# Kernel tuning notes

Measured on AMD Instinct MI355X. Metric: run time of the kernel, lower is better.

The kernel has to match this reference:

```python
import jax, jax.numpy as jnp
import numpy as np

N = 50000      # nodes
E = 800000     # edges in adj1/adj2 (avg degree 16)
ED = 400000    # edges after edge-drop
IN = 256       # input feature dim
H = 128        # hidden
H2 = 256       # 2*hidden
GATE = 64


def _xavier(key, shape):
    fan_in, fan_out = shape[0], shape[1]
    lim = np.sqrt(6.0 / (fan_in + fan_out)).astype(np.float32)
    return jax.random.uniform(key, shape, jnp.float32, -lim, lim)


def setup_inputs() -> dict:
    key = jax.random.key(0)
    ks = jax.random.split(key, 20)
    d = {}
    d["x1"] = jax.random.normal(ks[0], (N, IN), jnp.float32)
    d["x2"] = jax.random.normal(ks[1], (N, IN), jnp.float32)
    d["adj1_row"] = jax.random.randint(ks[2], (E,), 0, N, jnp.int32)
    d["adj1_col"] = jax.random.randint(ks[3], (E,), 0, N, jnp.int32)
    d["adj1_val"] = jax.random.uniform(ks[4], (E,), jnp.float32)
    d["adj2_row"] = jax.random.randint(ks[5], (E,), 0, N, jnp.int32)
    d["adj2_col"] = jax.random.randint(ks[6], (E,), 0, N, jnp.int32)
    d["adj2_val"] = jax.random.uniform(ks[7], (E,), jnp.float32)
    d["drop_row"] = jax.random.randint(ks[8], (ED,), 0, N, jnp.int32)
    d["drop_col"] = jax.random.randint(ks[9], (ED,), 0, N, jnp.int32)
    d["drop_val"] = jax.random.uniform(ks[10], (ED,), jnp.float32)
    d["deg"] = jax.random.uniform(ks[11], (N, 1), jnp.float32)
    # GCN layer 0: Linear(IN -> 2H) no bias in fc, plus GCN bias + PReLU
    d["W0"] = _xavier(ks[12], (IN, H2))
    d["b0"] = jnp.zeros((H2,), jnp.float32)
    d["a0"] = jnp.full((1,), 0.25, jnp.float32)  # PReLU param
    # GCN layer 1: Linear(2H -> H)
    d["W1"] = _xavier(ks[13], (H2, H))
    d["b1"] = jnp.zeros((H,), jnp.float32)
    d["a1"] = jnp.full((1,), 0.25, jnp.float32)
    # MLP gate
    d["G1w"] = _xavier(ks[14], (H, GATE))
    d["G1b"] = jnp.zeros((GATE,), jnp.float32)
    d["G2w"] = _xavier(ks[15], (H, GATE))
    d["G2b"] = jnp.zeros((GATE,), jnp.float32)
    d["G3w"] = _xavier(ks[16], (2 * GATE + 1, 1))
    d["G3b"] = jnp.zeros((1,), jnp.float32)
    return d


def _spmm(row, col, val, x, n):
    # sparse adj @ x : gather source features, scale by edge value, scatter-add to rows
    return jax.ops.segment_sum(val[:, None] * x[col], row, num_segments=n)


def _prelu(x, a):
    return jnp.where(x >= 0, x, a * x)


def reference(x1, x2, adj1_row, adj1_col, adj1_val, adj2_row, adj2_col, adj2_val,
              drop_row, drop_col, drop_val, deg,
              W0, b0, a0, W1, b1, a1, G1w, G1b, G2w, G2b, G3w, G3b):
    n = x1.shape[0]

    def gcn(x, row, col, val, W, b, a):
        return _prelu(_spmm(row, col, val, x @ W, n) + b, a)

    def branch(x, row, col, val):
        h = jax.nn.relu(gcn(x, row, col, val, W0, b0, a0))
        return gcn(h, row, col, val, W1, b1, a1)

    # dropout on x1/x2 is identity in eval mode
    h1 = branch(x1, adj1_row, adj1_col, adj1_val)
    h2 = branch(x2, adj1_row, adj1_col, adj1_val)
    h3 = branch(x1, adj2_row, adj2_col, adj2_val)
    h4 = branch(x1, drop_row, drop_col, drop_val)

    # MLP gate on detached h1, h3, deg
    z1 = jax.lax.stop_gradient(h1) @ G1w + G1b
    z2 = jax.lax.stop_gradient(h3) @ G2w + G2b
    w = jnp.concatenate([z1, z2, jax.lax.stop_gradient(deg)], axis=1)
    beta = jax.nn.sigmoid(w @ G3w + G3b)
    return (h1, h2, h3, h4, beta)
```

## Files before the change

### kernel.cpp

```cpp
#include <hip/hip_runtime.h>
#include <hip/hip_bf16.h>

#define H2C 256
#define HDC 128
#define GATEC 64
#define FBSH 9
#define NBF 320
#define EPB 8192
#define EPBH 2048
#define CAPB 10240

typedef unsigned short ushort_t;
typedef unsigned long long ull_t;
typedef __attribute__((ext_vector_type(8))) __bf16 bf16x8;
typedef __attribute__((ext_vector_type(4))) float f32x4;

__device__ inline float bf2f(unsigned short v) {
    union { unsigned u; float f; } t; t.u = ((unsigned)v) << 16; return t.f;
}
__device__ inline unsigned short f2bf(float v) {
    __hip_bfloat16 b = __float2bfloat16(v);
    return *reinterpret_cast<unsigned short*>(&b);
}

__device__ inline void gload_lds16(const void* g, void* l) {
    __builtin_amdgcn_global_load_lds(
        (const __attribute__((address_space(1))) unsigned int*)g,
        (__attribute__((address_space(3))) unsigned int*)l, 16, 0, 0);
}

__global__ __launch_bounds__(256)
void gemm_bf16_mfma(const ushort_t* __restrict__ A, const ushort_t* __restrict__ BT,
                    ushort_t* __restrict__ C, int M, int Nn, int K)
{
    __shared__ ushort_t Alds[128 * 64];
    __shared__ ushort_t Blds[128 * 64];
    const int tid  = threadIdx.x;
    const int w    = tid >> 6;
    const int lane = tid & 63;
    const int wr   = w >> 1;
    const int wc   = w & 1;
    const int bm   = blockIdx.y * 128;
    const int bn   = blockIdx.x * 128;

    f32x4 acc[4][4] = {};

    for (int k0 = 0; k0 < K; k0 += 64) {
        #pragma unroll
        for (int i = 0; i < 4; ++i) {
            const int lin = i * 256 + tid;
            const int r = lin >> 3, p = lin & 7;
            int rm = bm + r; if (rm >= M) rm = M - 1;
            const ushort_t* ga = A + (size_t)rm * K + k0 + ((p ^ (r & 7)) << 3);
            gload_lds16(ga, &Alds[i * 2048 + w * 512]);
        }
        #pragma unroll
        for (int i = 0; i < 4; ++i) {
            const int lin = i * 256 + tid;
            const int r = lin >> 3, p = lin & 7;
            const ushort_t* gb = BT + (size_t)(bn + r) * K + k0 + ((p ^ (r & 7)) << 3);
            gload_lds16(gb, &Blds[i * 2048 + w * 512]);
        }
        __syncthreads();
        #pragma unroll
        for (int kk = 0; kk < 2; ++kk) {
            bf16x8 af[4], bfr[4];
            #pragma unroll
            for (int m = 0; m < 4; ++m) {
                const int r = wr * 64 + m * 16 + (lane & 15);
                const int s = kk * 4 + (lane >> 4);
                af[m] = *reinterpret_cast<const bf16x8*>(&Alds[r * 64 + ((s ^ (r & 7)) << 3)]);
            }
            #pragma unroll
            for (int n = 0; n < 4; ++n) {
                const int r = wc * 64 + n * 16 + (lane & 15);
                const int s = kk * 4 + (lane >> 4);
                bfr[n] = *reinterpret_cast<const bf16x8*>(&Blds[r * 64 + ((s ^ (r & 7)) << 3)]);
            }
            #pragma unroll
            for (int m = 0; m < 4; ++m)
                #pragma unroll
                for (int n = 0; n < 4; ++n)
                    acc[m][n] = __builtin_amdgcn_mfma_f32_16x16x32_bf16(
                        af[m], bfr[n], acc[m][n], 0, 0, 0);
        }
        __syncthreads();
    }

    #pragma unroll
    for (int m = 0; m < 4; ++m) {
        const int row0 = bm + wr * 64 + m * 16 + ((lane >> 4) << 2);
        #pragma unroll
        for (int n = 0; n < 4; ++n) {
            const int col = bn + wc * 64 + n * 16 + (lane & 15);
            #pragma unroll
            for (int q = 0; q < 4; ++q) {
                const int row = row0 + q;
                if (row < M) C[(size_t)row * Nn + col] = f2bf(acc[m][n][q]);
            }
        }
    }
}

__global__ __launch_bounds__(256)
void gemm_xw_f32(const float* __restrict__ X1, const float* __restrict__ X2,
                 const ushort_t* __restrict__ BT, ushort_t* __restrict__ C,
                 int M, int Nn, int K, int Mh)
{
    __shared__ float    Af[128 * 32];
    __shared__ ushort_t Blds[128 * 32];
    const int tid  = threadIdx.x;
    const int w    = tid >> 6;
    const int lane = tid & 63;
    const int wr   = w >> 1;
    const int wc   = w & 1;
    const int bm   = blockIdx.y * 128;
    const int bn   = blockIdx.x * 128;

    f32x4 acc[4][4] = {};

    for (int k0 = 0; k0 < K; k0 += 32) {
        #pragma unroll
        for (int i = 0; i < 4; ++i) {
            const int lin = i * 256 + tid;
            const int r = lin >> 3, q = lin & 7;
            int rm = bm + r; if (rm >= M) rm = M - 1;
            const float* src = ((rm < Mh) ? X1 + (size_t)rm * K
                                          : X2 + (size_t)(rm - Mh) * K)
                               + k0 + ((q ^ (r & 7)) << 2);
            gload_lds16(src, &Af[i * 1024 + w * 256]);
        }
        #pragma unroll
        for (int i = 0; i < 2; ++i) {
            const int lin = i * 256 + tid;
            const int r = lin >> 2, q = lin & 3;
            const ushort_t* gb = BT + (size_t)(bn + r) * K + k0 + ((q ^ (r & 3)) << 3);
            gload_lds16(gb, &Blds[i * 2048 + w * 512]);
        }
        __syncthreads();
        {
            bf16x8 af[4], bfr[4];
            #pragma unroll
            for (int m = 0; m < 4; ++m) {
                const int r = wr * 64 + m * 16 + (lane & 15);
                const int s = lane >> 4;
                const int rx = r & 7;
                const float4 fa = *reinterpret_cast<const float4*>(
                    &Af[r * 32 + (((2 * s) ^ rx) << 2)]);
                const float4 fb = *reinterpret_cast<const float4*>(
                    &Af[r * 32 + (((2 * s + 1) ^ rx) << 2)]);
                ushort_t t[8] = {f2bf(fa.x), f2bf(fa.y), f2bf(fa.z), f2bf(fa.w),
                                 f2bf(fb.x), f2bf(fb.y), f2bf(fb.z), f2bf(fb.w)};
                af[m] = *reinterpret_cast<bf16x8*>(t);
            }
            #pragma unroll
            for (int n = 0; n < 4; ++n) {
                const int r = wc * 64 + n * 16 + (lane & 15);
                const int s = lane >> 4;
                bfr[n] = *reinterpret_cast<const bf16x8*>(&Blds[r * 32 + ((s ^ (r & 3)) << 3)]);
            }
            #pragma unroll
            for (int m = 0; m < 4; ++m)
                #pragma unroll
                for (int n = 0; n < 4; ++n)
                    acc[m][n] = __builtin_amdgcn_mfma_f32_16x16x32_bf16(
                        af[m], bfr[n], acc[m][n], 0, 0, 0);
        }
        __syncthreads();
    }

    #pragma unroll
    for (int m = 0; m < 4; ++m) {
        const int row0 = bm + wr * 64 + m * 16 + ((lane >> 4) << 2);
        #pragma unroll
        for (int n = 0; n < 4; ++n) {
            const int col = bn + wc * 64 + n * 16 + (lane & 15);
            #pragma unroll
            for (int q = 0; q < 4; ++q) {
                const int row = row0 + q;
                if (row < M) C[(size_t)row * Nn + col] = f2bf(acc[m][n][q]);
            }
        }
    }
}

__global__ __launch_bounds__(256)
void transpose2_f2bf_kernel(const float* __restrict__ W0, const float* __restrict__ W1,
                            ushort_t* __restrict__ W0T, ushort_t* __restrict__ W1T)
{
    int i = blockIdx.x * blockDim.x + threadIdx.x;
    if (i < H2C * H2C) {
        const int c = i / H2C, r = i % H2C;
        W0T[(size_t)c * H2C + r] = f2bf(W0[(size_t)r * H2C + c]);
    } else {
        i -= H2C * H2C;
        if (i < H2C * HDC) {
            const int c = i / H2C, r = i % H2C;
            W1T[(size_t)c * H2C + r] = f2bf(W1[(size_t)r * HDC + c]);
        }
    }
}

__global__ __launch_bounds__(256)
void bucket_hist_kernel(const int* __restrict__ r0, const int* __restrict__ r1_,
                        const int* __restrict__ rD, int E, int ED, int N,
                        int* __restrict__ bcnt)
{
    __shared__ int h[NBF];
    const int tid = threadIdx.x;
    for (int t = tid; t < NBF; t += 256) h[t] = 0;
    __syncthreads();
    const long long tot = 2LL * E + ED;
    const long long base = (long long)blockIdx.x * EPBH;
    #pragma unroll
    for (int k = 0; k < EPBH / 256; ++k) {
        const long long i = base + k * 256 + tid;
        if (i < tot) {
            int vr;
            if (i < E)            vr = r0[i];
            else if (i < 2LL * E) vr = N + r1_[i - E];
            else                  vr = 2 * N + rD[i - 2LL * E];
            atomicAdd(&h[vr >> FBSH], 1);
        }
    }
    __syncthreads();
    for (int t = tid; t < NBF; t += 256)
        if (h[t]) atomicAdd(&bcnt[t], h[t]);
}

__global__ void scan_buckets_kernel(const int* __restrict__ bcnt, int nbu, int tot,
                                    int* __restrict__ boff, int* __restrict__ gcur,
                                    int* __restrict__ g, int NR)
{
    if (threadIdx.x == 0) {
        int acc = 0;
        for (int t = 0; t < nbu; ++t) { boff[t] = acc; gcur[t] = acc; acc += bcnt[t]; }
        boff[nbu] = acc;
        g[NR] = tot;
    }
}

__global__ __launch_bounds__(256)
void bucket_stage_kernel(const int* __restrict__ r0, const int* __restrict__ c0, const float* __restrict__ v0,
                         const int* __restrict__ r1, const int* __restrict__ c1, const float* __restrict__ v1,
                         const int* __restrict__ rD, const int* __restrict__ cD, const float* __restrict__ vD,
                         int E, int ED, int N,
                         int* __restrict__ gcur, ull_t* __restrict__ stg)
{
    __shared__ int hcnt[NBF];
    __shared__ int hbase[NBF];
    const int tid = threadIdx.x;
    for (int t = tid; t < NBF; t += 256) hcnt[t] = 0;
    __syncthreads();
    const long long tot = 2LL * E + ED;
    const long long base = (long long)blockIdx.x * EPB;
    #pragma unroll
    for (int k = 0; k < EPB / 256; ++k) {
        const long long i = base + k * 256 + tid;
        if (i < tot) {
            int vr;
            if (i < E)            vr = r0[i];
            else if (i < 2LL * E) vr = N + r1[i - E];
            else                  vr = 2 * N + rD[i - 2LL * E];
            atomicAdd(&hcnt[vr >> FBSH], 1);
        }
    }
    __syncthreads();
    for (int t = tid; t < NBF; t += 256) {
        const int c = hcnt[t];
        hbase[t] = c ? atomicAdd(&gcur[t], c) : 0;
        hcnt[t] = 0;
    }
    __syncthreads();
    #pragma unroll
    for (int k = 0; k < EPB / 256; ++k) {
        const long long i = base + k * 256 + tid;
        if (i < tot) {
            int vr, cc; float vv;
            if (i < E)            { vr = r0[i];                 cc = c0[i];            vv = v0[i]; }
            else if (i < 2LL * E) { vr = N + r1[i - E];         cc = c1[i - E];        vv = v1[i - E]; }
            else                  { vr = 2 * N + rD[i - 2LL * E]; cc = cD[i - 2LL * E]; vv = vD[i - 2LL * E]; }
            const int fb = vr >> FBSH;
            const int p = hbase[fb] + atomicAdd(&hcnt[fb], 1);
            stg[p] = ((ull_t)(unsigned)vr << 32) | ((unsigned)cc << 16) | f2bf(vv);
        }
    }
}

__global__ __launch_bounds__(256)
void sort_bucket_kernel(const int* __restrict__ boff, int NR,
                        const ull_t* __restrict__ stg,
                        int* __restrict__ g, unsigned* __restrict__ ecv)
{
    __shared__ int hcnt[512];
    __shared__ int hscan[512];
    __shared__ unsigned pay[CAPB];
    const int b = blockIdx.x;
    const int r0 = b << FBSH;
    if (r0 >= NR) return;
    int r1 = r0 + (1 << FBSH); if (r1 > NR) r1 = NR;
    const int nrows = r1 - r0;
    const int base = boff[b], end = boff[b + 1];
    const int bsz = end - base;
    const int tid = threadIdx.x;
    hcnt[tid] = 0; hcnt[tid + 256] = 0;
    __syncthreads();
    for (int i = base + tid; i < end; i += 256)
        atomicAdd(&hcnt[(int)(stg[i] >> 32) - r0], 1);
    __syncthreads();
    hscan[tid] = hcnt[tid]; hscan[tid + 256] = hcnt[tid + 256];
    __syncthreads();
    for (int o = 1; o < 512; o <<= 1) {
        const int a0 = (tid >= o) ? hscan[tid - o] : 0;
        const int a1 = (tid + 256 >= o) ? hscan[tid + 256 - o] : 0;
        __syncthreads();
        hscan[tid] += a0; hscan[tid + 256] += a1;
        __syncthreads();
    }
    if (tid < nrows)       g[r0 + tid]       = base + hscan[tid] - hcnt[tid];
    if (tid + 256 < nrows) g[r0 + tid + 256] = base + hscan[tid + 256] - hcnt[tid + 256];
    hcnt[tid]       = hscan[tid] - hcnt[tid];
    hcnt[tid + 256] = hscan[tid + 256] - hcnt[tid + 256];
    __syncthreads();
    if (bsz <= CAPB) {
        for (int i = base + tid; i < end; i += 256) {
            const ull_t t = stg[i];
            const int p = atomicAdd(&hcnt[(int)(t >> 32) - r0], 1);
            pay[p] = (unsigned)t;
        }
        __syncthreads();
        for (int i = tid; i < bsz; i += 256)
            ecv[base + i] = pay[i];
    } else {
        for (int i = base + tid; i < end; i += 256) {
            const ull_t t = stg[i];
            const int p = atomicAdd(&hcnt[(int)(t >> 32) - r0], 1);
            ecv[base + p] = (unsigned)t;
        }
    }
}

__global__ __launch_bounds__(256)
void spmm_f256(const int* __restrict__ rp, const unsigned* __restrict__ ecv,
               const ushort_t* __restrict__ X, ushort_t* __restrict__ Y,
               const float* __restrict__ bias, const float* __restrict__ ap, int n)
{
    const int r = blockIdx.x * 4 + (threadIdx.x >> 6);
    if (r >= n) return;
    const int lane = threadIdx.x & 63;
    const int half = lane >> 5;
    const int l    = lane & 31;
    const int s = rp[r], e = rp[r + 1];
    float acc[8] = {};
    #pragma unroll 4
    for (int j = s + half; j < e; j += 2) {
        const unsigned ev = ecv[j];
        const float v = bf2f((ushort_t)ev);
        const uint4 x = *reinterpret_cast<const uint4*>(X + (size_t)(ev >> 16) * H2C + l * 8);
        acc[0] += v * bf2f((ushort_t)x.x); acc[1] += v * bf2f((ushort_t)(x.x >> 16));
        acc[2] += v * bf2f((ushort_t)x.y); acc[3] += v * bf2f((ushort_t)(x.y >> 16));
        acc[4] += v * bf2f((ushort_t)x.z); acc[5] += v * bf2f((ushort_t)(x.z >> 16));
        acc[6] += v * bf2f((ushort_t)x.w); acc[7] += v * bf2f((ushort_t)(x.w >> 16));
    }
    #pragma unroll
    for (int k = 0; k < 8; ++k) acc[k] += __shfl_xor(acc[k], 32);
    if (half == 0) {
        const float a = ap[0];
        const int f0 = l * 8;
        const float4 b0v = *reinterpret_cast<const float4*>(bias + f0);
        const float4 b1v = *reinterpret_cast<const float4*>(bias + f0 + 4);
        const float bb[8] = {b0v.x, b0v.y, b0v.z, b0v.w, b1v.x, b1v.y, b1v.z, b1v.w};
        unsigned o[4];
        #pragma unroll
        for (int k = 0; k < 8; k += 2) {
            float tx = acc[k] + bb[k];
            float ty = acc[k + 1] + bb[k + 1];
            tx = tx >= 0.f ? tx : a * tx;  ty = ty >= 0.f ? ty : a * ty;
            tx = fmaxf(tx, 0.f);           ty = fmaxf(ty, 0.f);
            o[k >> 1] = ((unsigned)f2bf(ty) << 16) | f2bf(tx);
        }
        *reinterpret_cast<uint4*>(Y + (size_t)r * H2C + f0) = make_uint4(o[0], o[1], o[2], o[3]);
    }
}

__global__ __launch_bounds__(256)
void spmm_f128(const int* __restrict__ rp, const unsigned* __restrict__ ecv,
               const ushort_t* __restrict__ X, float* __restrict__ Y,
               const float* __restrict__ bias, const float* __restrict__ ap, int n)
{
    const int r = blockIdx.x * 4 + (threadIdx.x >> 6);
    if (r >= n) return;
    const int lane = threadIdx.x & 63;
    const int q = lane >> 4;
    const int l = lane & 15;
    const int s = rp[r], e = rp[r + 1];
    float acc[8] = {};
    #pragma unroll 4
    for (int j = s + q; j < e; j += 4) {
        const unsigned ev = ecv[j];
        const float v = bf2f((ushort_t)ev);
        const uint4 x = *reinterpret_cast<const uint4*>(X + (size_t)(ev >> 16) * HDC + l * 8);
        acc[0] += v * bf2f((ushort_t)x.x); acc[1] += v * bf2f((ushort_t)(x.x >> 16));
        acc[2] += v * bf2f((ushort_t)x.y); acc[3] += v * bf2f((ushort_t)(x.y >> 16));
        acc[4] += v * bf2f((ushort_t)x.z); acc[5] += v * bf2f((ushort_t)(x.z >> 16));
        acc[6] += v * bf2f((ushort_t)x.w); acc[7] += v * bf2f((ushort_t)(x.w >> 16));
    }
    #pragma unroll
    for (int k = 0; k < 8; ++k) {
        acc[k] += __shfl_xor(acc[k], 16);
        acc[k] += __shfl_xor(acc[k], 32);
    }
    if (q == 0) {
        const float a = ap[0];
        const int f0 = l * 8;
        const float4 b0v = *reinterpret_cast<const float4*>(bias + f0);
        const float4 b1v = *reinterpret_cast<const float4*>(bias + f0 + 4);
        const float bb[8] = {b0v.x, b0v.y, b0v.z, b0v.w, b1v.x, b1v.y, b1v.z, b1v.w};
        float o[8];
        #pragma unroll
        for (int k = 0; k < 8; ++k) {
            float t = acc[k] + bb[k];
            o[k] = t >= 0.f ? t : a * t;
        }
        *reinterpret_cast<float4*>(Y + (size_t)r * HDC + f0)     = make_float4(o[0], o[1], o[2], o[3]);
        *reinterpret_cast<float4*>(Y + (size_t)r * HDC + f0 + 4) = make_float4(o[4], o[5], o[6], o[7]);
    }
}

__global__ __launch_bounds__(256)
void spmm_f128b(const int* __restrict__ rp, const unsigned* __restrict__ ecv,
                const ushort_t* __restrict__ X, float* __restrict__ out,
                const float* __restrict__ bias, const float* __restrict__ ap,
                int n3, int N)
{
    const int r = blockIdx.x * 4 + (threadIdx.x >> 6);
    if (r >= n3) return;
    const int reg = (r >= 2 * N) ? 2 : ((r >= N) ? 1 : 0);
    const ushort_t* Xs = X + (size_t)reg * N * HDC;
    float* Y = out + (size_t)(reg ? r + N : r) * HDC;
    const int lane = threadIdx.x & 63;
    const int q = lane >> 4;
    const int l = lane & 15;
    const int s = rp[r], e = rp[r + 1];
    float acc[8] = {};
    #pragma unroll 4
    for (int j = s + q; j < e; j += 4) {
        const unsigned ev = ecv[j];
        const float v = bf2f((ushort_t)ev);
        const uint4 x = *reinterpret_cast<const uint4*>(Xs + (size_t)(ev >> 16) * HDC + l * 8);
        acc[0] += v * bf2f((ushort_t)x.x); acc[1] += v * bf2f((ushort_t)(x.x >> 16));
        acc[2] += v * bf2f((ushort_t)x.y); acc[3] += v * bf2f((ushort_t)(x.y >> 16));
        acc[4] += v * bf2f((ushort_t)x.z); acc[5] += v * bf2f((ushort_t)(x.z >> 16));
        acc[6] += v * bf2f((ushort_t)x.w); acc[7] += v * bf2f((ushort_t)(x.w >> 16));
    }
    #pragma unroll
    for (int k = 0; k < 8; ++k) {
        acc[k] += __shfl_xor(acc[k], 16);
        acc[k] += __shfl_xor(acc[k], 32);
    }
    if (q == 0) {
        const float a = ap[0];
        const int f0 = l * 8;
        const float4 b0v = *reinterpret_cast<const float4*>(bias + f0);
        const float4 b1v = *reinterpret_cast<const float4*>(bias + f0 + 4);
        const float bb[8] = {b0v.x, b0v.y, b0v.z, b0v.w, b1v.x, b1v.y, b1v.z, b1v.w};
        float o[8];
        #pragma unroll
        for (int k = 0; k < 8; ++k) {
            float t = acc[k] + bb[k];
            o[k] = t >= 0.f ? t : a * t;
        }
        *reinterpret_cast<float4*>(Y + f0)     = make_float4(o[0], o[1], o[2], o[3]);
        *reinterpret_cast<float4*>(Y + f0 + 4) = make_float4(o[4], o[5], o[6], o[7]);
    }
}

__global__ void gate_pre_kernel(const float* __restrict__ G1w, const float* __restrict__ G1b,
                                const float* __restrict__ G2w, const float* __restrict__ G2b,
                                const float* __restrict__ G3w, const float* __restrict__ G3b,
                                float* __restrict__ U)
{
    const int h = threadIdx.x;
    float s1 = 0.f, s2 = 0.f;
    for (int g = 0; g < GATEC; ++g) {
        s1 += G1w[h * GATEC + g] * G3w[g];
        s2 += G2w[h * GATEC + g] * G3w[GATEC + g];
    }
    U[h] = s1;
    U[HDC + h] = s2;
    if (h == 0) {
        float c = G3b[0];
        for (int g = 0; g < GATEC; ++g)
            c += G1b[g] * G3w[g] + G2b[g] * G3w[GATEC + g];
        U[2 * HDC] = c;
        U[2 * HDC + 1] = G3w[2 * GATEC];
    }
}

__global__ __launch_bounds__(256)
void beta_kernel(const float* __restrict__ h1, const float* __restrict__ h3,
                 const float* __restrict__ deg, const float* __restrict__ U,
                 float* __restrict__ beta, int n)
{
    const int i = blockIdx.x * blockDim.x + threadIdx.x;
    if (i >= n) return;
    const float c = U[2 * HDC], wd = U[2 * HDC + 1];
    float s = c + wd * deg[i];
    const float4* h1p = reinterpret_cast<const float4*>(h1 + (size_t)i * HDC);
    const float4* h3p = reinterpret_cast<const float4*>(h3 + (size_t)i * HDC);
    const float4* u1p = reinterpret_cast<const float4*>(U);
    const float4* u2p = reinterpret_cast<const float4*>(U + HDC);
    #pragma unroll 8
    for (int j = 0; j < HDC / 4; ++j) {
        const float4 a = h1p[j], b = u1p[j];
        s += a.x * b.x + a.y * b.y + a.z * b.z + a.w * b.w;
        const float4 a2 = h3p[j], b2 = u2p[j];
        s += a2.x * b2.x + a2.y * b2.y + a2.z * b2.z + a2.w * b2.w;
    }
    beta[i] = 1.f / (1.f + expf(-s));
}

extern "C" void kernel_launch(void* const* d_in, const int* in_sizes, int n_in,
                              void* d_out, int out_size, void* d_ws, size_t ws_size,
                              hipStream_t stream)
{
    const float* x1  = (const float*)d_in[0];
    const float* x2  = (const float*)d_in[1];
    const int*   a1r = (const int*)d_in[2];
    const int*   a1c = (const int*)d_in[3];
    const float* a1v = (const float*)d_in[4];
    const int*   a2r = (const int*)d_in[5];
    const int*   a2c = (const int*)d_in[6];
    const float* a2v = (const float*)d_in[7];
    const int*   dr  = (const int*)d_in[8];
    const int*   dc  = (const int*)d_in[9];
    const float* dv  = (const float*)d_in[10];
    const float* deg = (const float*)d_in[11];
    const float* W0  = (const float*)d_in[12];
    const float* b0  = (const float*)d_in[13];
    const float* a0  = (const float*)d_in[14];
    const float* W1  = (const float*)d_in[15];
    const float* b1  = (const float*)d_in[16];
    const float* a1p = (const float*)d_in[17];
    const float* G1w = (const float*)d_in[18];
    const float* G1b = (const float*)d_in[19];
    const float* G2w = (const float*)d_in[20];
    const float* G2b = (const float*)d_in[21];
    const float* G3w = (const float*)d_in[22];
    const float* G3b = (const float*)d_in[23];

    const int E  = in_sizes[2];
    const int ED = in_sizes[8];
    const int N  = in_sizes[11];
    const int IN = in_sizes[0] / N;
    const long long TOT = 2LL * E + ED;
    const int NR  = 3 * N;
    const int NBUSED = (NR + (1 << FBSH) - 1) >> FBSH;

    auto pad = [](size_t b) { return (b + 255) & ~(size_t)255; };

    size_t need_b = pad((size_t)2 * N * H2C * 2)
                  + pad((size_t)3 * N * H2C * 2)
                  + pad((size_t)3 * N * HDC * 2)
                  + pad((size_t)H2C * H2C * 2) + pad((size_t)HDC * H2C * 2) + pad(258 * 4)
                  + pad((size_t)(NR + 1) * 4) + pad(NBF * 4) + pad((NBF + 1) * 4) + pad(NBF * 4)
                  + pad((size_t)TOT * 4)
                  + pad((size_t)TOT * 8);
    const bool batched = (ws_size >= need_b);

    char* base = (char*)d_ws;
    size_t off = 0;
    auto alloc = [&](size_t bytes) -> char* {
        char* p = base + off;
        off += (bytes + 255) & ~(size_t)255;
        return p;
    };
    ushort_t* XW12b = (ushort_t*)alloc((size_t)2 * N * H2C * 2);
    ull_t* stg; ushort_t *Bb, *Cb;
    if (batched) {
        char* R = alloc((size_t)3 * N * H2C * 2);
        Bb = (ushort_t*)R;
        Cb = (ushort_t*)alloc((size_t)3 * N * HDC * 2);
        stg = (ull_t*)alloc((size_t)TOT * 8);
    } else {
        char* R = alloc((size_t)N * H2C * 2 + (size_t)N * HDC * 2);
        stg = (ull_t*)R;
        Bb  = (ushort_t*)R;
        Cb  = (ushort_t*)(R + (size_t)N * H2C * 2);
    }
    ushort_t* W0T  = (ushort_t*)alloc((size_t)H2C * H2C * 2);
    ushort_t* W1T  = (ushort_t*)alloc((size_t)HDC * H2C * 2);
    float*    U    = (float*)alloc(258 * 4);
    int*  g       = (int*)alloc((size_t)(NR + 1) * 4);
    int*  bcnt    = (int*)alloc(NBF * 4);
    int*  boff    = (int*)alloc((NBF + 1) * 4);
    int*  gcur    = (int*)alloc(NBF * 4);
    unsigned* ecv = (unsigned*)alloc((size_t)TOT * 4);

    float* out  = (float*)d_out;
    float* h1   = out;
    float* h2   = out + 1 * (size_t)N * HDC;
    float* h3   = out + 2 * (size_t)N * HDC;
    float* h4   = out + 3 * (size_t)N * HDC;
    float* beta = out + 4 * (size_t)N * HDC;

    gate_pre_kernel<<<1, HDC, 0, stream>>>(G1w, G1b, G2w, G2b, G3w, G3b, U);
    transpose2_f2bf_kernel<<<dim3((H2C * H2C + H2C * HDC + 255) / 256), 256, 0, stream>>>(
        W0, W1, W0T, W1T);

    hipMemsetAsync(bcnt, 0, NBF * 4, stream);
    bucket_hist_kernel<<<dim3((unsigned)((TOT + EPBH - 1) / EPBH)), 256, 0, stream>>>(
        a1r, a2r, dr, E, ED, N, bcnt);
    scan_buckets_kernel<<<1, 64, 0, stream>>>(bcnt, NBUSED, (int)TOT, boff, gcur, g, NR);

    bucket_stage_kernel<<<dim3((unsigned)((TOT + EPB - 1) / EPB)), 256, 0, stream>>>(
        a1r, a1c, a1v, a2r, a2c, a2v, dr, dc, dv, E, ED, N, gcur, stg);
    sort_bucket_kernel<<<dim3(NBUSED), 256, 0, stream>>>(boff, NR, stg, g, ecv);

    gemm_xw_f32<<<dim3(H2C / 128, (2 * N + 127) / 128), 256, 0, stream>>>(
        x1, x2, W0T, XW12b, 2 * N, H2C, IN, N);

    const ushort_t* XW1b = XW12b;
    const ushort_t* XW2b = XW12b + (size_t)N * H2C;

    if (batched) {
        spmm_f256<<<dim3((NR + 3) / 4), 256, 0, stream>>>(g, ecv, XW1b, Bb, b0, a0, NR);
        gemm_bf16_mfma<<<dim3(HDC / 128, (NR + 127) / 128), 256, 0, stream>>>(
            Bb, W1T, Cb, NR, HDC, H2C);
        spmm_f128b<<<dim3((NR + 3) / 4), 256, 0, stream>>>(g, ecv, Cb, out, b1, a1p, NR, N);
        spmm_f256<<<dim3((N + 3) / 4), 256, 0, stream>>>(g, ecv, XW2b, Bb, b0, a0, N);
        gemm_bf16_mfma<<<dim3(HDC / 128, (N + 127) / 128), 256, 0, stream>>>(
            Bb, W1T, Cb, N, HDC, H2C);
        spmm_f128<<<dim3((N + 3) / 4), 256, 0, stream>>>(g, ecv, Cb, h2, b1, a1p, N);
    } else {
        const int* rp1 = g;
        const int* rp2 = g + N;
        const int* rpD = g + 2 * N;
        auto run_branch = [&](const int* rp, const ushort_t* Xsrc, float* hout) {
            spmm_f256<<<dim3((N + 3) / 4), 256, 0, stream>>>(rp, ecv, Xsrc, Bb, b0, a0, N);
            gemm_bf16_mfma<<<dim3(HDC / 128, (N + 127) / 128), 256, 0, stream>>>(
                Bb, W1T, Cb, N, HDC, H2C);
            spmm_f128<<<dim3((N + 3) / 4), 256, 0, stream>>>(rp, ecv, Cb, hout, b1, a1p, N);
        };
        run_branch(rp1, XW1b, h1);
        run_branch(rp2, XW1b, h3);
        run_branch(rpD, XW1b, h4);
        run_branch(rp1, XW2b, h2);
    }

    beta_kernel<<<dim3((N + 255) / 256), 256, 0, stream>>>(h1, h3, deg, U, beta, N);
}
```

Baseline: 511.5 us.

## Batch all four branches, drop histogram pass, convert A to bf16 at load

```diff
diff --git a/kernel.cpp b/kernel.cpp
--- a/kernel.cpp
+++ b/kernel.cpp
@@ -7,7 +7,7 @@
 #define FBSH 9
 #define NBF 320
 #define EPB 8192
-#define EPBH 2048
+#define CAPS 10240
 #define CAPB 10240
 
 typedef unsigned short ushort_t;
@@ -107,8 +107,8 @@
                  const ushort_t* __restrict__ BT, ushort_t* __restrict__ C,
                  int M, int Nn, int K, int Mh)
 {
-    __shared__ float    Af[128 * 32];
-    __shared__ ushort_t Blds[128 * 32];
+    __shared__ ushort_t Alds[128 * 64];
+    __shared__ ushort_t Blds[128 * 64];
     const int tid  = threadIdx.x;
     const int w    = tid >> 6;
     const int lane = tid & 63;
@@ -119,45 +119,45 @@
 
     f32x4 acc[4][4] = {};
 
-    for (int k0 = 0; k0 < K; k0 += 32) {
+    for (int k0 = 0; k0 < K; k0 += 64) {
         #pragma unroll
         for (int i = 0; i < 4; ++i) {
             const int lin = i * 256 + tid;
-            const int r = lin >> 3, q = lin & 7;
+            const int r = lin >> 3, p = lin & 7;
             int rm = bm + r; if (rm >= M) rm = M - 1;
-            const float* src = ((rm < Mh) ? X1 + (size_t)rm * K
-                                          : X2 + (size_t)(rm - Mh) * K)
-                               + k0 + ((q ^ (r & 7)) << 2);
-            gload_lds16(src, &Af[i * 1024 + w * 256]);
-        }
-        #pragma unroll
-        for (int i = 0; i < 2; ++i) {
+            const float* ga = ((rm < Mh) ? X1 + (size_t)rm * K
+                                         : X2 + (size_t)(rm - Mh) * K) + k0 + p * 8;
+            const float4 fa = *reinterpret_cast<const float4*>(ga);
+            const float4 fb = *reinterpret_cast<const float4*>(ga + 4);
+            ushort_t* dst = &Alds[r * 64 + ((p ^ (r & 7)) << 3)];
+            ushort4 o0, o1;
+            o0.x = f2bf(fa.x); o0.y = f2bf(fa.y); o0.z = f2bf(fa.z); o0.w = f2bf(fa.w);
+            o1.x = f2bf(fb.x); o1.y = f2bf(fb.y); o1.z = f2bf(fb.z); o1.w = f2bf(fb.w);
+            *reinterpret_cast<ushort4*>(dst)     = o0;
+            *reinterpret_cast<ushort4*>(dst + 4) = o1;
+        }
+        #pragma unroll
+        for (int i = 0; i < 4; ++i) {
             const int lin = i * 256 + tid;
-            const int r = lin >> 2, q = lin & 3;
-            const ushort_t* gb = BT + (size_t)(bn + r) * K + k0 + ((q ^ (r & 3)) << 3);
+            const int r = lin >> 3, p = lin & 7;
+            const ushort_t* gb = BT + (size_t)(bn + r) * K + k0 + ((p ^ (r & 7)) << 3);
             gload_lds16(gb, &Blds[i * 2048 + w * 512]);
         }
         __syncthreads();
-        {
+        #pragma unroll
+        for (int kk = 0; kk < 2; ++kk) {
             bf16x8 af[4], bfr[4];
             #pragma unroll
             for (int m = 0; m < 4; ++m) {
                 const int r = wr * 64 + m * 16 + (lane & 15);
-                const int s = lane >> 4;
-                const int rx = r & 7;
-                const float4 fa = *reinterpret_cast<const float4*>(
-                    &Af[r * 32 + (((2 * s) ^ rx) << 2)]);
-                const float4 fb = *reinterpret_cast<const float4*>(
-                    &Af[r * 32 + (((2 * s + 1) ^ rx) << 2)]);
-                ushort_t t[8] = {f2bf(fa.x), f2bf(fa.y), f2bf(fa.z), f2bf(fa.w),
-                                 f2bf(fb.x), f2bf(fb.y), f2bf(fb.z), f2bf(fb.w)};
-                af[m] = *reinterpret_cast<bf16x8*>(t);
+                const int s = kk * 4 + (lane >> 4);
+                af[m] = *reinterpret_cast<const bf16x8*>(&Alds[r * 64 + ((s ^ (r & 7)) << 3)]);
             }
             #pragma unroll
             for (int n = 0; n < 4; ++n) {
                 const int r = wc * 64 + n * 16 + (lane & 15);
-                const int s = lane >> 4;
-                bfr[n] = *reinterpret_cast<const bf16x8*>(&Blds[r * 32 + ((s ^ (r & 3)) << 3)]);
+                const int s = kk * 4 + (lane >> 4);
+                bfr[n] = *reinterpret_cast<const bf16x8*>(&Blds[r * 64 + ((s ^ (r & 7)) << 3)]);
             }
             #pragma unroll
             for (int m = 0; m < 4; ++m)
@@ -201,43 +201,10 @@
     }
 }
 
-__global__ __launch_bounds__(256)
-void bucket_hist_kernel(const int* __restrict__ r0, const int* __restrict__ r1_,
-                        const int* __restrict__ rD, int E, int ED, int N,
-                        int* __restrict__ bcnt)
-{
-    __shared__ int h[NBF];
-    const int tid = threadIdx.x;
-    for (int t = tid; t < NBF; t += 256) h[t] = 0;
-    __syncthreads();
-    const long long tot = 2LL * E + ED;
-    const long long base = (long long)blockIdx.x * EPBH;
-    #pragma unroll
-    for (int k = 0; k < EPBH / 256; ++k) {
-        const long long i = base + k * 256 + tid;
-        if (i < tot) {
-            int vr;
-            if (i < E)            vr = r0[i];
-            else if (i < 2LL * E) vr = N + r1_[i - E];
-            else                  vr = 2 * N + rD[i - 2LL * E];
-            atomicAdd(&h[vr >> FBSH], 1);
-        }
-    }
-    __syncthreads();
-    for (int t = tid; t < NBF; t += 256)
-        if (h[t]) atomicAdd(&bcnt[t], h[t]);
-}
-
-__global__ void scan_buckets_kernel(const int* __restrict__ bcnt, int nbu, int tot,
-                                    int* __restrict__ boff, int* __restrict__ gcur,
-                                    int* __restrict__ g, int NR)
-{
-    if (threadIdx.x == 0) {
-        int acc = 0;
-        for (int t = 0; t < nbu; ++t) { boff[t] = acc; gcur[t] = acc; acc += bcnt[t]; }
-        boff[nbu] = acc;
-        g[NR] = tot;
-    }
+__global__ void init_gcur_kernel(int* __restrict__ gcur)
+{
+    const int t = blockIdx.x * blockDim.x + threadIdx.x;
+    if (t < NBF) gcur[t] = t * CAPS;
 }
 
 __global__ __launch_bounds__(256)
@@ -282,8 +249,23 @@
             else                  { vr = 2 * N + rD[i - 2LL * E]; cc = cD[i - 2LL * E]; vv = vD[i - 2LL * E]; }
             const int fb = vr >> FBSH;
             const int p = hbase[fb] + atomicAdd(&hcnt[fb], 1);
-            stg[p] = ((ull_t)(unsigned)vr << 32) | ((unsigned)cc << 16) | f2bf(vv);
-        }
+            if (p < (fb + 1) * CAPS)
+                stg[p] = ((ull_t)(unsigned)vr << 32) | ((unsigned)cc << 16) | f2bf(vv);
+        }
+    }
+}
+
+__global__ void scan_buckets_kernel(const int* __restrict__ gcur, int nbu, int tot,
+                                    int* __restrict__ boff, int* __restrict__ g, int NR)
+{
+    if (threadIdx.x == 0) {
+        int acc = 0;
+        for (int t = 0; t < nbu; ++t) {
+            boff[t] = acc;
+            acc += gcur[t] - t * CAPS;
+        }
+        boff[nbu] = acc;
+        g[NR] = tot;
     }
 }
 
@@ -300,13 +282,14 @@
     if (r0 >= NR) return;
     int r1 = r0 + (1 << FBSH); if (r1 > NR) r1 = NR;
     const int nrows = r1 - r0;
-    const int base = boff[b], end = boff[b + 1];
-    const int bsz = end - base;
+    const int obase = boff[b];
+    const int bsz   = boff[b + 1] - obase;
+    const int sbase = b * CAPS;
     const int tid = threadIdx.x;
     hcnt[tid] = 0; hcnt[tid + 256] = 0;
     __syncthreads();
-    for (int i = base + tid; i < end; i += 256)
-        atomicAdd(&hcnt[(int)(stg[i] >> 32) - r0], 1);
+    for (int i = tid; i < bsz; i += 256)
+        atomicAdd(&hcnt[(int)(stg[sbase + i] >> 32) - r0], 1);
     __syncthreads();
     hscan[tid] = hcnt[tid]; hscan[tid + 256] = hcnt[tid + 256];
     __syncthreads();
@@ -317,27 +300,19 @@
         hscan[tid] += a0; hscan[tid + 256] += a1;
         __syncthreads();
     }
-    if (tid < nrows)       g[r0 + tid]       = base + hscan[tid] - hcnt[tid];
-    if (tid + 256 < nrows) g[r0 + tid + 256] = base + hscan[tid + 256] - hcnt[tid + 256];
+    if (tid < nrows)       g[r0 + tid]       = obase + hscan[tid] - hcnt[tid];
+    if (tid + 256 < nrows) g[r0 + tid + 256] = obase + hscan[tid + 256] - hcnt[tid + 256];
     hcnt[tid]       = hscan[tid] - hcnt[tid];
     hcnt[tid + 256] = hscan[tid + 256] - hcnt[tid + 256];
     __syncthreads();
-    if (bsz <= CAPB) {
-        for (int i = base + tid; i < end; i += 256) {
-            const ull_t t = stg[i];
-            const int p = atomicAdd(&hcnt[(int)(t >> 32) - r0], 1);
-            pay[p] = (unsigned)t;
-        }
-        __syncthreads();
-        for (int i = tid; i < bsz; i += 256)
-            ecv[base + i] = pay[i];
-    } else {
-        for (int i = base + tid; i < end; i += 256) {
-            const ull_t t = stg[i];
-            const int p = atomicAdd(&hcnt[(int)(t >> 32) - r0], 1);
-            ecv[base + p] = (unsigned)t;
-        }
-    }
+    for (int i = tid; i < bsz; i += 256) {
+        const ull_t t = stg[sbase + i];
+        const int p = atomicAdd(&hcnt[(int)(t >> 32) - r0], 1);
+        pay[p] = (unsigned)t;
+    }
+    __syncthreads();
+    for (int i = tid; i < bsz; i += 256)
+        ecv[obase + i] = pay[i];
 }
 
 __global__ __launch_bounds__(256)
@@ -384,6 +359,52 @@
 }
 
 __global__ __launch_bounds__(256)
+void spmm_f256q(const int* __restrict__ rp, const unsigned* __restrict__ ecv,
+                const ushort_t* __restrict__ XW1, const ushort_t* __restrict__ XW2,
+                ushort_t* __restrict__ Bb, const float* __restrict__ bias,
+                const float* __restrict__ ap, int NR, int N)
+{
+    const int vr = blockIdx.x * 4 + (threadIdx.x >> 6);
+    if (vr >= NR + N) return;
+    const int rr = (vr >= NR) ? vr - NR : vr;
+    const ushort_t* X = (vr >= NR) ? XW2 : XW1;
+    const int lane = threadIdx.x & 63;
+    const int half = lane >> 5;
+    const int l    = lane & 31;
+    const int s = rp[rr], e = rp[rr + 1];
+    float acc[8] = {};
+    #pragma unroll 4
+    for (int j = s + half; j < e; j += 2) {
+        const unsigned ev = ecv[j];
+        const float v = bf2f((ushort_t)ev);
+        const uint4 x = *reinterpret_cast<const uint4*>(X + (size_t)(ev >> 16) * H2C + l * 8);
+        acc[0] += v * bf2f((ushort_t)x.x); acc[1] += v * bf2f((ushort_t)(x.x >> 16));
+        acc[2] += v * bf2f((ushort_t)x.y); acc[3] += v * bf2f((ushort_t)(x.y >> 16));
+        acc[4] += v * bf2f((ushort_t)x.z); acc[5] += v * bf2f((ushort_t)(x.z >> 16));
+        acc[6] += v * bf2f((ushort_t)x.w); acc[7] += v * bf2f((ushort_t)(x.w >> 16));
+    }
+    #pragma unroll
+    for (int k = 0; k < 8; ++k) acc[k] += __shfl_xor(acc[k], 32);
+    if (half == 0) {
+        const float a = ap[0];
+        const int f0 = l * 8;
+        const float4 b0v = *reinterpret_cast<const float4*>(bias + f0);
+        const float4 b1v = *reinterpret_cast<const float4*>(bias + f0 + 4);
+        const float bb[8] = {b0v.x, b0v.y, b0v.z, b0v.w, b1v.x, b1v.y, b1v.z, b1v.w};
+        unsigned o[4];
+        #pragma unroll
+        for (int k = 0; k < 8; k += 2) {
+            float tx = acc[k] + bb[k];
+            float ty = acc[k + 1] + bb[k + 1];
+            tx = tx >= 0.f ? tx : a * tx;  ty = ty >= 0.f ? ty : a * ty;
+            tx = fmaxf(tx, 0.f);           ty = fmaxf(ty, 0.f);
+            o[k >> 1] = ((unsigned)f2bf(ty) << 16) | f2bf(tx);
+        }
+        *reinterpret_cast<uint4*>(Bb + (size_t)vr * H2C + f0) = make_uint4(o[0], o[1], o[2], o[3]);
+    }
+}
+
+__global__ __launch_bounds__(256)
 void spmm_f128(const int* __restrict__ rp, const unsigned* __restrict__ ecv,
                const ushort_t* __restrict__ X, float* __restrict__ Y,
                const float* __restrict__ bias, const float* __restrict__ ap, int n)
@@ -428,26 +449,28 @@
 }
 
 __global__ __launch_bounds__(256)
-void spmm_f128b(const int* __restrict__ rp, const unsigned* __restrict__ ecv,
-                const ushort_t* __restrict__ X, float* __restrict__ out,
+void spmm_f128q(const int* __restrict__ rp, const unsigned* __restrict__ ecv,
+                const ushort_t* __restrict__ Cb, float* __restrict__ out,
                 const float* __restrict__ bias, const float* __restrict__ ap,
-                int n3, int N)
-{
-    const int r = blockIdx.x * 4 + (threadIdx.x >> 6);
-    if (r >= n3) return;
-    const int reg = (r >= 2 * N) ? 2 : ((r >= N) ? 1 : 0);
-    const ushort_t* Xs = X + (size_t)reg * N * HDC;
-    float* Y = out + (size_t)(reg ? r + N : r) * HDC;
+                int NR, int N)
+{
+    const int vr = blockIdx.x * 4 + (threadIdx.x >> 6);
+    if (vr >= NR + N) return;
+    const int reg = (vr >= NR) ? 3 : ((vr >= 2 * N) ? 2 : ((vr >= N) ? 1 : 0));
+    const int rr = (reg == 3) ? vr - NR : vr;
+    const int orow = (reg == 0) ? vr : ((reg == 3) ? vr - 2 * N : vr + N);
+    float* Y = out + (size_t)orow * HDC;
+    const ushort_t* Xbase = Cb + (size_t)reg * N * HDC;
     const int lane = threadIdx.x & 63;
     const int q = lane >> 4;
     const int l = lane & 15;
-    const int s = rp[r], e = rp[r + 1];
+    const int s = rp[rr], e = rp[rr + 1];
     float acc[8] = {};
     #pragma unroll 4
     for (int j = s + q; j < e; j += 4) {
         const unsigned ev = ecv[j];
         const float v = bf2f((ushort_t)ev);
-        const uint4 x = *reinterpret_cast<const uint4*>(Xs + (size_t)(ev >> 16) * HDC + l * 8);
+        const uint4 x = *reinterpret_cast<const uint4*>(Xbase + (size_t)(ev >> 16) * HDC + l * 8);
         acc[0] += v * bf2f((ushort_t)x.x); acc[1] += v * bf2f((ushort_t)(x.x >> 16));
         acc[2] += v * bf2f((ushort_t)x.y); acc[3] += v * bf2f((ushort_t)(x.y >> 16));
         acc[4] += v * bf2f((ushort_t)x.z); acc[5] += v * bf2f((ushort_t)(x.z >> 16));
@@ -555,18 +578,19 @@
     const int IN = in_sizes[0] / N;
     const long long TOT = 2LL * E + ED;
     const int NR  = 3 * N;
+    const int N4  = 4 * N;
     const int NBUSED = (NR + (1 << FBSH) - 1) >> FBSH;
 
     auto pad = [](size_t b) { return (b + 255) & ~(size_t)255; };
-
-    size_t need_b = pad((size_t)2 * N * H2C * 2)
-                  + pad((size_t)3 * N * H2C * 2)
-                  + pad((size_t)3 * N * HDC * 2)
-                  + pad((size_t)H2C * H2C * 2) + pad((size_t)HDC * H2C * 2) + pad(258 * 4)
-                  + pad((size_t)(NR + 1) * 4) + pad(NBF * 4) + pad((NBF + 1) * 4) + pad(NBF * 4)
-                  + pad((size_t)TOT * 4)
-                  + pad((size_t)TOT * 8);
-    const bool batched = (ws_size >= need_b);
+    const size_t fixed = pad((size_t)2 * N * H2C * 2)
+                       + pad((size_t)H2C * H2C * 2) + pad((size_t)HDC * H2C * 2)
+                       + pad(258 * 4) + pad((size_t)(NR + 1) * 4)
+                       + pad((NBF + 1) * 4) + pad(NBF * 4)
+                       + pad((size_t)TOT * 4)
+                       + pad((size_t)NBF * CAPS * 8);
+    const size_t need4 = fixed + pad((size_t)N4 * H2C * 2) + pad((size_t)N4 * HDC * 2);
+    const size_t need3 = fixed + pad((size_t)NR * H2C * 2) + pad((size_t)NR * HDC * 2);
+    const int tier = (ws_size >= need4) ? 1 : ((ws_size >= need3) ? 2 : 3);
 
     char* base = (char*)d_ws;
     size_t off = 0;
@@ -577,22 +601,26 @@
     };
     ushort_t* XW12b = (ushort_t*)alloc((size_t)2 * N * H2C * 2);
     ull_t* stg; ushort_t *Bb, *Cb;
-    if (batched) {
-        char* R = alloc((size_t)3 * N * H2C * 2);
-        Bb = (ushort_t*)R;
-        Cb = (ushort_t*)alloc((size_t)3 * N * HDC * 2);
-        stg = (ull_t*)alloc((size_t)TOT * 8);
+    if (tier == 1) {
+        Bb  = (ushort_t*)alloc((size_t)N4 * H2C * 2);
+        Cb  = (ushort_t*)alloc((size_t)N4 * HDC * 2);
+        stg = (ull_t*)alloc((size_t)NBF * CAPS * 8);
+    } else if (tier == 2) {
+        Bb  = (ushort_t*)alloc((size_t)NR * H2C * 2);
+        Cb  = (ushort_t*)alloc((size_t)NR * HDC * 2);
+        stg = (ull_t*)alloc((size_t)NBF * CAPS * 8);
     } else {
-        char* R = alloc((size_t)N * H2C * 2 + (size_t)N * HDC * 2);
+        char* R = alloc((size_t)NBF * CAPS * 8);
         stg = (ull_t*)R;
         Bb  = (ushort_t*)R;
         Cb  = (ushort_t*)(R + (size_t)N * H2C * 2);
+        if ((size_t)NBF * CAPS * 8 < (size_t)N * (H2C + HDC) * 2)
+            alloc((size_t)N * (H2C + HDC) * 2 - (size_t)NBF * CAPS * 8);
     }
     ushort_t* W0T  = (ushort_t*)alloc((size_t)H2C * H2C * 2);
     ushort_t* W1T  = (ushort_t*)alloc((size_t)HDC * H2C * 2);
     float*    U    = (float*)alloc(258 * 4);
     int*  g       = (int*)alloc((size_t)(NR + 1) * 4);
-    int*  bcnt    = (int*)alloc(NBF * 4);
     int*  boff    = (int*)alloc((NBF + 1) * 4);
     int*  gcur    = (int*)alloc(NBF * 4);
     unsigned* ecv = (unsigned*)alloc((size_t)TOT * 4);
@@ -608,13 +636,10 @@
     transpose2_f2bf_kernel<<<dim3((H2C * H2C + H2C * HDC + 255) / 256), 256, 0, stream>>>(
         W0, W1, W0T, W1T);
 
-    hipMemsetAsync(bcnt, 0, NBF * 4, stream);
-    bucket_hist_kernel<<<dim3((unsigned)((TOT + EPBH - 1) / EPBH)), 256, 0, stream>>>(
-        a1r, a2r, dr, E, ED, N, bcnt);
-    scan_buckets_kernel<<<1, 64, 0, stream>>>(bcnt, NBUSED, (int)TOT, boff, gcur, g, NR);
-
+    init_gcur_kernel<<<dim3(2), 256, 0, stream>>>(gcur);
     bucket_stage_kernel<<<dim3((unsigned)((TOT + EPB - 1) / EPB)), 256, 0, stream>>>(
         a1r, a1c, a1v, a2r, a2c, a2v, dr, dc, dv, E, ED, N, gcur, stg);
+    scan_buckets_kernel<<<1, 64, 0, stream>>>(gcur, NBUSED, (int)TOT, boff, g, NR);
     sort_bucket_kernel<<<dim3(NBUSED), 256, 0, stream>>>(boff, NR, stg, g, ecv);
 
     gemm_xw_f32<<<dim3(H2C / 128, (2 * N + 127) / 128), 256, 0, stream>>>(
@@ -623,29 +648,35 @@
     const ushort_t* XW1b = XW12b;
     const ushort_t* XW2b = XW12b + (size_t)N * H2C;
 
-    if (batched) {
+    if (tier == 1) {
+        spmm_f256q<<<dim3((N4 + 3) / 4), 256, 0, stream>>>(
+            g, ecv, XW1b, XW2b, Bb, b0, a0, NR, N);
+        gemm_bf16_mfma<<<dim3(HDC / 128, (N4 + 127) / 128), 256, 0, stream>>>(
+            Bb, W1T, Cb, N4, HDC, H2C);
+        spmm_f128q<<<dim3((N4 + 3) / 4), 256, 0, stream>>>(
+            g, ecv, Cb, out, b1, a1p, NR, N);
+    } else if (tier == 2) {
         spmm_f256<<<dim3((NR + 3) / 4), 256, 0, stream>>>(g, ecv, XW1b, Bb, b0, a0, NR);
         gemm_bf16_mfma<<<dim3(HDC / 128, (NR + 127) / 128), 256, 0, stream>>>(
             Bb, W1T, Cb, NR, HDC, H2C);
-        spmm_f128b<<<dim3((NR + 3) / 4), 256, 0, stream>>>(g, ecv, Cb, out, b1, a1p, NR, N);
+        spmm_f128<<<dim3((N + 3) / 4), 256, 0, stream>>>(g, ecv, Cb, h1, b1, a1p, N);
+        spmm_f128<<<dim3((N + 3) / 4), 256, 0, stream>>>(g + N, ecv, Cb + (size_t)N * HDC, h3, b1, a1p, N);
+        spmm_f128<<<dim3((N + 3) / 4), 256, 0, stream>>>(g + 2 * N, ecv, Cb + (size_t)2 * N * HDC, h4, b1, a1p, N);
         spmm_f256<<<dim3((N + 3) / 4), 256, 0, stream>>>(g, ecv, XW2b, Bb, b0, a0, N);
         gemm_bf16_mfma<<<dim3(HDC / 128, (N + 127) / 128), 256, 0, stream>>>(
             Bb, W1T, Cb, N, HDC, H2C);
         spmm_f128<<<dim3((N + 3) / 4), 256, 0, stream>>>(g, ecv, Cb, h2, b1, a1p, N);
     } else {
-        const int* rp1 = g;
-        const int* rp2 = g + N;
-        const int* rpD = g + 2 * N;
         auto run_branch = [&](const int* rp, const ushort_t* Xsrc, float* hout) {
             spmm_f256<<<dim3((N + 3) / 4), 256, 0, stream>>>(rp, ecv, Xsrc, Bb, b0, a0, N);
             gemm_bf16_mfma<<<dim3(HDC / 128, (N + 127) / 128), 256, 0, stream>>>(
                 Bb, W1T, Cb, N, HDC, H2C);
             spmm_f128<<<dim3((N + 3) / 4), 256, 0, stream>>>(rp, ecv, Cb, hout, b1, a1p, N);
         };
-        run_branch(rp1, XW1b, h1);
-        run_branch(rp2, XW1b, h3);
-        run_branch(rpD, XW1b, h4);
-        run_branch(rp1, XW2b, h2);
+        run_branch(g, XW1b, h1);
+        run_branch(g + N, XW1b, h3);
+        run_branch(g + 2 * N, XW1b, h4);
+        run_branch(g, XW2b, h2);
     }
 
     beta_kernel<<<dim3((N + 255) / 256), 256, 0, stream>>>(h1, h3, deg, U, beta, N);
```

Result: faster. 480.7 us (-6.0%).
